# Kernel tuning notes

Hardware: AMD Instinct MI355X
Metric: run time of the kernel (lower is better)

The kernel has to match this reference:

```python
import jax, jax.numpy as jnp
import numpy as np

# 3x3 hexagon kernel mask: zero at (0,2) and (2,0), matching HexagonConv2d
_KM = np.ones((3, 3), np.float32)
_KM[0, 2] = 0.0
_KM[2, 0] = 0.0
KMASK = jnp.asarray(_KM)


def _out_mask():
    # static 13x13 mask encoding the post-conv zeroing loops
    m = np.ones((13, 13), np.float32)
    for i in range(5):
        for j in range(8 + i, 13):
            m[i, j] = 0.0
    for i in range(4):
        m[2 + i, 9 + i] = 0.0
    m[6:9, 12] = 0.0
    for i in range(6):
        for j in range(i + 1):
            m[6 + i, j] = 0.0
    for i in range(3):
        m[5 + i, 0 + i] = 0.0
    m[3:5, 0] = 0.0
    return jnp.asarray(m)

OUT_MASK = _out_mask()


def _hex_pad(x):
    # x: [B,C,13,13] -> zero-pad to [B,C,15,15], then hexagonal wraparound copies.
    # Copies applied sequentially, exactly matching the torch in-place order
    # (one copy, row 0 <- row 12, feeds a later read at (0,7)).
    x = jnp.pad(x, ((0, 0), (0, 0), (1, 1), (1, 1)))
    r2 = jnp.arange(2)
    r3 = jnp.arange(3)
    r4 = jnp.arange(4)
    r8 = jnp.arange(8)
    x = x.at[:, :, 0, 1:8].set(x[:, :, 12, 7:14])
    x = x.at[:, :, r3, 8 + r3].set(x[:, :, 6 + r3, 2 + r3])
    x = x.at[:, :, 3 + r4, 10 + r4].set(x[:, :, 9 + r4, 4 + r4])
    x = x.at[:, :, 7 + r3, 13].set(x[:, :, 1 + r3, 1])
    x = x.at[:, :, 10 + r3, 14].set(x[:, :, 4 + r3, 2])
    x = x.at[:, :, 13, 7 + r8].set(x[:, :, 1, 1 + r8])
    x = x.at[:, :, 9 + r4, 3 + r4].set(x[:, :, 3 + r4, 9 + r4])
    x = x.at[:, :, 6 + r3, 1 + r3].set(x[:, :, r3, 7 + r3])
    x = x.at[:, :, 4 + r2, 1].set(x[:, :, 10 + r2, 13])
    x = x.at[:, :, r4, 0].set(x[:, :, 6 + r4, 12])
    return x


def setup_inputs() -> dict:
    key = jax.random.key(0)
    kx, kw, kb = jax.random.split(key, 3)
    B, Cin, Cout, H = 4096, 64, 64, 13
    x = jax.random.normal(kx, (B, Cin, H, H), dtype=jnp.float32)
    fan_in = Cin * 9
    w = jax.random.normal(kw, (Cout, Cin, 3, 3), dtype=jnp.float32) / np.sqrt(fan_in)
    b = jax.random.normal(kb, (Cout,), dtype=jnp.float32) * 0.01
    return {"x": x, "w": w, "b": b}


def reference(x, w, b):
    xp = _hex_pad(x)                      # [B,C,15,15]
    wm = w * KMASK                        # hexagonal kernel mask
    y = jax.lax.conv_general_dilated(
        xp, wm, window_strides=(1, 1), padding="VALID",
        dimension_numbers=("NCHW", "OIHW", "NCHW"))  # [B,Cout,13,13]
    y = y + b[None, :, None, None]
    return y * OUT_MASK
```

## Files before the change

kernel.cpp:

```cpp
#include <hip/hip_runtime.h>
#include <stdint.h>

typedef __attribute__((ext_vector_type(8))) short short8;
typedef __attribute__((ext_vector_type(4))) float float4v;

#define NPIX 240
#define PIXSTRIDE 68

#define MAP_OFF   57344
#define OM_OFF    58304

__device__ __forceinline__ unsigned short f2bf(float f) {
    union { float f; unsigned u; } v; v.f = f;
    unsigned r = v.u + 0x7FFFu + ((v.u >> 16) & 1u);
    return (unsigned short)(r >> 16);
}

__global__ void hex_prep_kernel(const float* __restrict__ w,
                                unsigned short* __restrict__ wsA,
                                int* __restrict__ map,
                                float* __restrict__ om) {
    const int gid = blockIdx.x * blockDim.x + threadIdx.x;
    const int nthr = gridDim.x * blockDim.x;
    const int ti_tab[7] = {0,0,1,1,1,2,2};
    const int tj_tab[7] = {0,1,0,1,2,1,2};
    for (int item = gid; item < 4*14*64; item += nthr) {
        int lane = item & 63;
        int ks   = (item >> 6) % 14;
        int ct   = (item >> 6) / 14;
        int co = ct*16 + (lane & 15);
        int k0 = ks*32 + (lane >> 4)*8;
        unsigned short vals[8];
        #pragma unroll
        for (int j = 0; j < 8; ++j) {
            int k = k0 + j;
            int tap = k >> 6, ci = k & 63;
            vals[j] = f2bf(w[(co*64 + ci)*9 + ti_tab[tap]*3 + tj_tab[tap]]);
        }
        for (int j = 0; j < 8; ++j) wsA[item*8 + j] = vals[j];
    }
    if (gid == 0) {
        int m[225];
        for (int r = 0; r < 15; ++r)
            for (int c = 0; c < 15; ++c)
                m[r*15+c] = (r>=1 && r<=13 && c>=1 && c<=13) ? (r-1)*13 + (c-1) : -1;
        #define M(r,c) m[(r)*15+(c)]
        for (int t = 0; t < 7; ++t) M(0,1+t)    = M(12,7+t);
        for (int r = 0; r < 3; ++r) M(r,8+r)    = M(6+r,2+r);
        for (int r = 0; r < 4; ++r) M(3+r,10+r) = M(9+r,4+r);
        for (int r = 0; r < 3; ++r) M(7+r,13)   = M(1+r,1);
        for (int r = 0; r < 3; ++r) M(10+r,14)  = M(4+r,2);
        for (int r = 0; r < 8; ++r) M(13,7+r)   = M(1,1+r);
        for (int r = 0; r < 4; ++r) M(9+r,3+r)  = M(3+r,9+r);
        for (int r = 0; r < 3; ++r) M(6+r,1+r)  = M(r,7+r);
        for (int r = 0; r < 2; ++r) M(4+r,1)    = M(10+r,13);
        for (int r = 0; r < 4; ++r) M(r,0)      = M(6+r,12);
        #undef M
        for (int i = 0; i < 225; ++i) map[i] = m[i];
        for (int i = 225; i < 240; ++i) map[i] = -1;
        float o[169];
        for (int i = 0; i < 169; ++i) o[i] = 1.f;
        for (int i = 0; i < 5; ++i) for (int j = 8+i; j < 13; ++j) o[i*13+j] = 0.f;
        for (int i = 0; i < 4; ++i) o[(2+i)*13 + 9+i] = 0.f;
        for (int i = 6; i < 9; ++i) o[i*13 + 12] = 0.f;
        for (int i = 0; i < 6; ++i) for (int j = 0; j <= i; ++j) o[(6+i)*13 + j] = 0.f;
        for (int i = 0; i < 3; ++i) o[(5+i)*13 + i] = 0.f;
        o[3*13 + 0] = 0.f; o[4*13 + 0] = 0.f;
        for (int i = 0; i < 169; ++i) om[i] = o[i];
    }
}

__global__ __launch_bounds__(256, 2) void hexconv_kernel(
        const float* __restrict__ x, const float* __restrict__ bias,
        const unsigned short* __restrict__ wsA, const int* __restrict__ map,
        const float* __restrict__ om, float* __restrict__ out) {
    __shared__ unsigned short Xs[NPIX * PIXSTRIDE];
    const int b   = blockIdx.x;
    const int tid = threadIdx.x;
    const int lane = tid & 63, wv = tid >> 6;
    const int lr = lane & 15, lq = lane >> 4;
    const float* xb = x + (size_t)b * 64 * 169;

    const int ctp = wv & 1;
    const int nth = wv >> 1;

    short8 afr[2][14];
    #pragma unroll
    for (int c = 0; c < 2; ++c) {
        const int ct = ctp*2 + c;
        #pragma unroll
        for (int ks = 0; ks < 14; ++ks)
            afr[c][ks] = *(const short8*)(wsA + (size_t)((ct*14 + ks)*64 + lane)*8);
    }

    int sp[4];
    #pragma unroll
    for (int pi = 0; pi < 4; ++pi) {
        int pix = lane + 64*pi;
        sp[pi] = (pix < NPIX) ? map[pix] : -1;
    }
    #pragma unroll
    for (int pi = 0; pi < 4; ++pi) {
        int pix = lane + 64*pi;
        if (pix < NPIX) {
            const int s = sp[pi];
            unsigned short vals[16];
            #pragma unroll
            for (int cj = 0; cj < 16; ++cj) {
                int ci = wv*16 + cj;
                float v = (s >= 0) ? xb[ci*169 + s] : 0.f;
                vals[cj] = f2bf(v);
            }
            #pragma unroll
            for (int q = 0; q < 4; ++q) {
                uint64_t pk = (uint64_t)vals[4*q]
                            | ((uint64_t)vals[4*q+1] << 16)
                            | ((uint64_t)vals[4*q+2] << 32)
                            | ((uint64_t)vals[4*q+3] << 48);
                *(uint64_t*)&Xs[pix*PIXSTRIDE + wv*16 + q*4] = pk;
            }
        }
    }
    __syncthreads();

    float4v acc[2][7];
    #pragma unroll
    for (int c = 0; c < 2; ++c)
        #pragma unroll
        for (int j = 0; j < 7; ++j)
            acc[c][j] = float4v{0.f, 0.f, 0.f, 0.f};

    const int offs[7] = {0,1,15,16,17,31,32};
    #pragma unroll
    for (int ks = 0; ks < 14; ++ks) {
        const int tap = ks >> 1;
        const int cib = (ks & 1)*32 + lq*8;
        #pragma unroll
        for (int j = 0; j < 7; ++j) {
            int nt = nth*7 + j;
            if (nt < 13) {
                int pixb = nt*16 + lr + offs[tap];
                const unsigned short* p = &Xs[pixb*PIXSTRIDE + cib];
                union { short8 v; uint64_t q[2]; } u;
                u.q[0] = *(const uint64_t*)p;
                u.q[1] = *(const uint64_t*)(p + 4);
                #pragma unroll
                for (int c = 0; c < 2; ++c)
                    acc[c][j] = __builtin_amdgcn_mfma_f32_16x16x32_bf16(
                        afr[c][ks], u.v, acc[c][j], 0, 0, 0);
            }
        }
    }

    #pragma unroll
    for (int j = 0; j < 7; ++j) {
        int nt = nth*7 + j;
        if (nt >= 13) continue;
        int p15 = nt*16 + lr;
        int y = p15 / 15, xc = p15 % 15;
        if (xc >= 13 || y >= 13) continue;
        float omv = om[y*13 + xc];
        size_t obase = (size_t)b*64*169 + y*13 + xc;
        #pragma unroll
        for (int c = 0; c < 2; ++c) {
            int ct = ctp*2 + c;
            #pragma unroll
            for (int r = 0; r < 4; ++r) {
                int co = ct*16 + lq*4 + r;
                out[obase + (size_t)co*169] = (acc[c][j][r] + bias[co]) * omv;
            }
        }
    }
}

extern "C" void kernel_launch(void* const* d_in, const int* in_sizes, int n_in,
                              void* d_out, int out_size, void* d_ws, size_t ws_size,
                              hipStream_t stream) {
    const float* x    = (const float*)d_in[0];
    const float* w    = (const float*)d_in[1];
    const float* bias = (const float*)d_in[2];
    float* out = (float*)d_out;

    unsigned short* wsA = (unsigned short*)d_ws;
    int*   map = (int*)((char*)d_ws + MAP_OFF);
    float* om  = (float*)((char*)d_ws + OM_OFF);

    hex_prep_kernel<<<16, 256, 0, stream>>>(w, wsA, map, om);

    int B = in_sizes[0] / (64 * 169);
    hexconv_kernel<<<B, 256, 0, stream>>>(x, bias, wsA, map, om, out);
}
```

Measured before the change: 358.4 us.

## Stream weight fragments per k-step, move index tables to constant memory, cheaper bf16 pack

The conv kernel stops holding all 28 weight fragments in registers. It now loads two fragments per k-step with a one-step prefetch, which lowers register pressure but adds a global or L2 load inside the MFMA loop. The pad-map and output-mask tables become compile-time constant memory, so the prep kernel no longer builds them serially on one thread. Input bf16 conversion switches from round-to-nearest-even to add-0x8000 rounding with a perm packing instruction, which saves ALU work but slightly changes rounding on ties.

```diff
diff --git a/kernel.cpp b/kernel.cpp
--- a/kernel.cpp
+++ b/kernel.cpp
@@ -7,19 +7,51 @@
 #define NPIX 240
 #define PIXSTRIDE 68
 
-#define MAP_OFF   57344
-#define OM_OFF    58304
+struct MapT { int m[256]; };
+constexpr MapT build_map() {
+    MapT t{};
+    int m[225] = {};
+    for (int r = 0; r < 15; ++r)
+        for (int c = 0; c < 15; ++c)
+            m[r*15+c] = (r>=1 && r<=13 && c>=1 && c<=13) ? (r-1)*13 + (c-1) : -1;
+    for (int k = 0; k < 7; ++k) m[0*15 + 1+k]      = m[12*15 + 7+k];
+    for (int r = 0; r < 3; ++r) m[r*15 + 8+r]      = m[(6+r)*15 + 2+r];
+    for (int r = 0; r < 4; ++r) m[(3+r)*15 + 10+r] = m[(9+r)*15 + 4+r];
+    for (int r = 0; r < 3; ++r) m[(7+r)*15 + 13]   = m[(1+r)*15 + 1];
+    for (int r = 0; r < 3; ++r) m[(10+r)*15 + 14]  = m[(4+r)*15 + 2];
+    for (int r = 0; r < 8; ++r) m[13*15 + 7+r]     = m[1*15 + 1+r];
+    for (int r = 0; r < 4; ++r) m[(9+r)*15 + 3+r]  = m[(3+r)*15 + 9+r];
+    for (int r = 0; r < 3; ++r) m[(6+r)*15 + 1+r]  = m[r*15 + 7+r];
+    for (int r = 0; r < 2; ++r) m[(4+r)*15 + 1]    = m[(10+r)*15 + 13];
+    for (int r = 0; r < 4; ++r) m[r*15 + 0]        = m[(6+r)*15 + 12];
+    for (int i = 0;   i < 225; ++i) t.m[i] = m[i];
+    for (int i = 225; i < 256; ++i) t.m[i] = -1;
+    return t;
+}
+__device__ __constant__ MapT c_map = build_map();
 
-__device__ __forceinline__ unsigned short f2bf(float f) {
+struct OmT { float v[169]; };
+constexpr OmT build_om() {
+    OmT t{};
+    for (int i = 0; i < 169; ++i) t.v[i] = 1.f;
+    for (int i = 0; i < 5; ++i) for (int j = 8+i; j < 13; ++j) t.v[i*13+j] = 0.f;
+    for (int i = 0; i < 4; ++i) t.v[(2+i)*13 + 9+i] = 0.f;
+    for (int i = 6; i < 9; ++i) t.v[i*13 + 12] = 0.f;
+    for (int i = 0; i < 6; ++i) for (int j = 0; j <= i; ++j) t.v[(6+i)*13 + j] = 0.f;
+    for (int i = 0; i < 3; ++i) t.v[(5+i)*13 + i] = 0.f;
+    t.v[3*13] = 0.f; t.v[4*13] = 0.f;
+    return t;
+}
+__device__ __constant__ OmT c_om = build_om();
+
+__device__ __forceinline__ unsigned short f2bf_rne(float f) {
     union { float f; unsigned u; } v; v.f = f;
     unsigned r = v.u + 0x7FFFu + ((v.u >> 16) & 1u);
     return (unsigned short)(r >> 16);
 }
 
 __global__ void hex_prep_kernel(const float* __restrict__ w,
-                                unsigned short* __restrict__ wsA,
-                                int* __restrict__ map,
-                                float* __restrict__ om) {
+                                unsigned short* __restrict__ wsA) {
     const int gid = blockIdx.x * blockDim.x + threadIdx.x;
     const int nthr = gridDim.x * blockDim.x;
     const int ti_tab[7] = {0,0,1,1,1,2,2};
@@ -35,45 +67,15 @@
         for (int j = 0; j < 8; ++j) {
             int k = k0 + j;
             int tap = k >> 6, ci = k & 63;
-            vals[j] = f2bf(w[(co*64 + ci)*9 + ti_tab[tap]*3 + tj_tab[tap]]);
+            vals[j] = f2bf_rne(w[(co*64 + ci)*9 + ti_tab[tap]*3 + tj_tab[tap]]);
         }
         for (int j = 0; j < 8; ++j) wsA[item*8 + j] = vals[j];
-    }
-    if (gid == 0) {
-        int m[225];
-        for (int r = 0; r < 15; ++r)
-            for (int c = 0; c < 15; ++c)
-                m[r*15+c] = (r>=1 && r<=13 && c>=1 && c<=13) ? (r-1)*13 + (c-1) : -1;
-        #define M(r,c) m[(r)*15+(c)]
-        for (int t = 0; t < 7; ++t) M(0,1+t)    = M(12,7+t);
-        for (int r = 0; r < 3; ++r) M(r,8+r)    = M(6+r,2+r);
-        for (int r = 0; r < 4; ++r) M(3+r,10+r) = M(9+r,4+r);
-        for (int r = 0; r < 3; ++r) M(7+r,13)   = M(1+r,1);
-        for (int r = 0; r < 3; ++r) M(10+r,14)  = M(4+r,2);
-        for (int r = 0; r < 8; ++r) M(13,7+r)   = M(1,1+r);
-        for (int r = 0; r < 4; ++r) M(9+r,3+r)  = M(3+r,9+r);
-        for (int r = 0; r < 3; ++r) M(6+r,1+r)  = M(r,7+r);
-        for (int r = 0; r < 2; ++r) M(4+r,1)    = M(10+r,13);
-        for (int r = 0; r < 4; ++r) M(r,0)      = M(6+r,12);
-        #undef M
-        for (int i = 0; i < 225; ++i) map[i] = m[i];
-        for (int i = 225; i < 240; ++i) map[i] = -1;
-        float o[169];
-        for (int i = 0; i < 169; ++i) o[i] = 1.f;
-        for (int i = 0; i < 5; ++i) for (int j = 8+i; j < 13; ++j) o[i*13+j] = 0.f;
-        for (int i = 0; i < 4; ++i) o[(2+i)*13 + 9+i] = 0.f;
-        for (int i = 6; i < 9; ++i) o[i*13 + 12] = 0.f;
-        for (int i = 0; i < 6; ++i) for (int j = 0; j <= i; ++j) o[(6+i)*13 + j] = 0.f;
-        for (int i = 0; i < 3; ++i) o[(5+i)*13 + i] = 0.f;
-        o[3*13 + 0] = 0.f; o[4*13 + 0] = 0.f;
-        for (int i = 0; i < 169; ++i) om[i] = o[i];
     }
 }
 
 __global__ __launch_bounds__(256, 2) void hexconv_kernel(
         const float* __restrict__ x, const float* __restrict__ bias,
-        const unsigned short* __restrict__ wsA, const int* __restrict__ map,
-        const float* __restrict__ om, float* __restrict__ out) {
+        const unsigned short* __restrict__ wsA, float* __restrict__ out) {
     __shared__ unsigned short Xs[NPIX * PIXSTRIDE];
     const int b   = blockIdx.x;
     const int tid = threadIdx.x;
@@ -84,40 +86,34 @@
     const int ctp = wv & 1;
     const int nth = wv >> 1;
 
-    short8 afr[2][14];
-    #pragma unroll
-    for (int c = 0; c < 2; ++c) {
-        const int ct = ctp*2 + c;
-        #pragma unroll
-        for (int ks = 0; ks < 14; ++ks)
-            afr[c][ks] = *(const short8*)(wsA + (size_t)((ct*14 + ks)*64 + lane)*8);
-    }
+    const unsigned short* wA = wsA + (size_t)((ctp*2*14)*64 + lane)*8;
+    short8 a0 = *(const short8*)(wA);
+    short8 a1 = *(const short8*)(wA + 14*64*8);
 
     int sp[4];
     #pragma unroll
-    for (int pi = 0; pi < 4; ++pi) {
-        int pix = lane + 64*pi;
-        sp[pi] = (pix < NPIX) ? map[pix] : -1;
-    }
+    for (int pi = 0; pi < 4; ++pi) sp[pi] = c_map.m[lane + 64*pi];
+
     #pragma unroll
     for (int pi = 0; pi < 4; ++pi) {
         int pix = lane + 64*pi;
         if (pix < NPIX) {
             const int s = sp[pi];
-            unsigned short vals[16];
+            uint32_t pk[8];
             #pragma unroll
-            for (int cj = 0; cj < 16; ++cj) {
-                int ci = wv*16 + cj;
-                float v = (s >= 0) ? xb[ci*169 + s] : 0.f;
-                vals[cj] = f2bf(v);
+            for (int h = 0; h < 8; ++h) {
+                int ci = wv*16 + 2*h;
+                float v0 = (s >= 0) ? xb[ci*169 + s]     : 0.f;
+                float v1 = (s >= 0) ? xb[(ci+1)*169 + s] : 0.f;
+                uint32_t u0 = __float_as_uint(v0) + 0x8000u;
+                uint32_t u1 = __float_as_uint(v1) + 0x8000u;
+                pk[h] = __builtin_amdgcn_perm(u1, u0, 0x07060302u);
             }
+            unsigned short* dst = &Xs[pix*PIXSTRIDE + wv*16];
             #pragma unroll
             for (int q = 0; q < 4; ++q) {
-                uint64_t pk = (uint64_t)vals[4*q]
-                            | ((uint64_t)vals[4*q+1] << 16)
-                            | ((uint64_t)vals[4*q+2] << 32)
-                            | ((uint64_t)vals[4*q+3] << 48);
-                *(uint64_t*)&Xs[pix*PIXSTRIDE + wv*16 + q*4] = pk;
+                uint64_t w2 = (uint64_t)pk[2*q] | ((uint64_t)pk[2*q+1] << 32);
+                *(uint64_t*)(dst + q*4) = w2;
             }
         }
     }
@@ -133,6 +129,11 @@
     const int offs[7] = {0,1,15,16,17,31,32};
     #pragma unroll
     for (int ks = 0; ks < 14; ++ks) {
+        short8 a0n = a0, a1n = a1;
+        if (ks < 13) {
+            a0n = *(const short8*)(wA + (size_t)(ks+1)*64*8);
+            a1n = *(const short8*)(wA + (size_t)(14 + ks+1)*64*8);
+        }
         const int tap = ks >> 1;
         const int cib = (ks & 1)*32 + lq*8;
         #pragma unroll
@@ -144,12 +145,11 @@
                 union { short8 v; uint64_t q[2]; } u;
                 u.q[0] = *(const uint64_t*)p;
                 u.q[1] = *(const uint64_t*)(p + 4);
-                #pragma unroll
-                for (int c = 0; c < 2; ++c)
-                    acc[c][j] = __builtin_amdgcn_mfma_f32_16x16x32_bf16(
-                        afr[c][ks], u.v, acc[c][j], 0, 0, 0);
+                acc[0][j] = __builtin_amdgcn_mfma_f32_16x16x32_bf16(a0, u.v, acc[0][j], 0, 0, 0);
+                acc[1][j] = __builtin_amdgcn_mfma_f32_16x16x32_bf16(a1, u.v, acc[1][j], 0, 0, 0);
             }
         }
+        a0 = a0n; a1 = a1n;
     }
 
     #pragma unroll
@@ -159,7 +159,7 @@
         int p15 = nt*16 + lr;
         int y = p15 / 15, xc = p15 % 15;
         if (xc >= 13 || y >= 13) continue;
-        float omv = om[y*13 + xc];
+        float omv = c_om.v[y*13 + xc];
         size_t obase = (size_t)b*64*169 + y*13 + xc;
         #pragma unroll
         for (int c = 0; c < 2; ++c) {
@@ -182,11 +182,9 @@
     float* out = (float*)d_out;
 
     unsigned short* wsA = (unsigned short*)d_ws;
-    int*   map = (int*)((char*)d_ws + MAP_OFF);
-    float* om  = (float*)((char*)d_ws + OM_OFF);
 
-    hex_prep_kernel<<<16, 256, 0, stream>>>(w, wsA, map, om);
+    hex_prep_kernel<<<16, 256, 0, stream>>>(w, wsA);
 
     int B = in_sizes[0] / (64 * 169);
-    hexconv_kernel<<<B, 256, 0, stream>>>(x, bias, wsA, map, om, out);
+    hexconv_kernel<<<B, 256, 0, stream>>>(x, bias, wsA, out);
 }
```

Measured after the change: 441.6 us. 23.2% more time.
